# Kernel optimization log

Measured on AMD Instinct MI355X. Metric: run time of the kernel, lower is better.

Reference implementation:

```python
import jax, jax.numpy as jnp
import numpy as np

HIDDEN = 2048
NUM_HEADS = 8
NUM_KV_HEADS = 4
HEAD_DIM = 256
N_REP = NUM_HEADS // NUM_KV_HEADS
EPS = 1e-6


def setup_inputs() -> dict:
    key = jax.random.key(0)
    ks = jax.random.split(key, 5)
    B, L = 2, 2048
    hidden_states = jax.random.normal(ks[0], (B, L, HIDDEN), dtype=jnp.float32)
    q_w = jax.random.normal(ks[1], (NUM_HEADS * HEAD_DIM, HIDDEN), dtype=jnp.float32) * 0.02
    k_w = jax.random.normal(ks[2], (NUM_KV_HEADS * HEAD_DIM, HIDDEN), dtype=jnp.float32) * 0.02
    v_w = jax.random.normal(ks[3], (NUM_KV_HEADS * HEAD_DIM, HIDDEN), dtype=jnp.float32) * 0.02
    o_w = jax.random.normal(ks[4], (HIDDEN, NUM_HEADS * HEAD_DIM), dtype=jnp.float32) * 0.02
    qnorm_w = jnp.ones((HEAD_DIM,), dtype=jnp.float32)
    knorm_w = jnp.ones((HEAD_DIM,), dtype=jnp.float32)
    return {"hidden_states": hidden_states, "q_w": q_w, "k_w": k_w, "v_w": v_w,
            "o_w": o_w, "qnorm_w": qnorm_w, "knorm_w": knorm_w}


def _rmsnorm(x, w):
    # RMSNorm over last dim (head_dim)
    var = jnp.mean(jnp.square(x), axis=-1, keepdims=True)
    return x * jax.lax.rsqrt(var + EPS) * w


def reference(hidden_states, q_w, k_w, v_w, o_w, qnorm_w, knorm_w):
    B, L, H = hidden_states.shape
    scale = HEAD_DIM ** -0.5
    # projections (Linear without bias: x @ W.T)
    q = (hidden_states @ q_w.T).reshape(B, L, NUM_HEADS, HEAD_DIM)
    k = (hidden_states @ k_w.T).reshape(B, L, NUM_KV_HEADS, HEAD_DIM)
    v = (hidden_states @ v_w.T).reshape(B, L, NUM_KV_HEADS, HEAD_DIM)
    # QK-norm on head_dim
    q = _rmsnorm(q, qnorm_w)
    k = _rmsnorm(k, knorm_w)
    # [B, heads, L, d]
    q = q.transpose(0, 2, 1, 3)
    k = k.transpose(0, 2, 1, 3)
    v = v.transpose(0, 2, 1, 3)
    # GQA expand kv heads: [B, kv, L, d] -> [B, kv*n_rep, L, d]
    k = jnp.repeat(k, N_REP, axis=1)
    v = jnp.repeat(v, N_REP, axis=1)
    # scores [B, h, q, k]
    scores = jnp.einsum('bhqd,bhkd->bhqk', q, k) * scale
    causal = jnp.triu(jnp.ones((L, L), dtype=bool), k=1)
    scores = jnp.where(causal, -jnp.inf, scores)
    probs = jax.nn.softmax(scores, axis=-1)
    out = jnp.einsum('bhqk,bhkd->bhqd', probs, v)
    out = out.transpose(0, 2, 1, 3).reshape(B, L, NUM_HEADS * HEAD_DIM)
    return out @ o_w.T
```

## Files before the change

kernel.cpp:

```cpp
#include <hip/hip_runtime.h>

typedef __bf16 bf16;
typedef __attribute__((ext_vector_type(4))) float f32x4;
typedef __attribute__((ext_vector_type(8))) __bf16 bf16x8;
typedef __attribute__((ext_vector_type(4))) __bf16 bf16x4;

#define HIDDEN 2048
#define L_SEQ 2048
#define NHEADS 8
#define NKV 4
#define HDIM 256

__device__ __forceinline__ void gload16(const bf16* g, void* l) {
  __builtin_amdgcn_global_load_lds((const __attribute__((address_space(1))) void*)g,
                                   (__attribute__((address_space(3))) void*)l, 16, 0, 0);
}

__global__ __launch_bounds__(256) void cast_bf16_kernel(const float* __restrict__ in,
                                                        bf16* __restrict__ out, int n4) {
  int i = blockIdx.x * 256 + threadIdx.x;
  if (i >= n4) return;
  float4 v = ((const float4*)in)[i];
  bf16x4 o;
  o[0] = (bf16)v.x; o[1] = (bf16)v.y; o[2] = (bf16)v.z; o[3] = (bf16)v.w;
  ((bf16x4*)out)[i] = o;
}

template <int OUT_BF16>
__global__ __launch_bounds__(256) void gemm_bt(const bf16* __restrict__ A,
                                               const bf16* __restrict__ B,
                                               void* __restrict__ C,
                                               int M, int N, int K) {
  __shared__ __attribute__((aligned(16))) bf16 As[128 * 64];
  __shared__ __attribute__((aligned(16))) bf16 Bs[128 * 64];
  const int tid = threadIdx.x;
  const int lane = tid & 63;
  const int wid = tid >> 6;
  const int m0 = blockIdx.y * 128;
  const int n0 = blockIdx.x * 128;
  const int wm = (wid >> 1) * 64;
  const int wn = (wid & 1) * 64;

  const int srow = tid >> 3;
  const int scolb = (tid & 7) * 16;

  f32x4 acc[4][4];
#pragma unroll
  for (int i = 0; i < 4; ++i)
#pragma unroll
    for (int j = 0; j < 4; ++j) acc[i][j] = (f32x4){0.f, 0.f, 0.f, 0.f};

  for (int k0 = 0; k0 < K; k0 += 64) {
    __syncthreads();
#pragma unroll
    for (int c = 0; c < 4; ++c) {
      int row = c * 32 + srow;
      int gcol = (scolb ^ ((row & 7) << 4)) >> 1;
      gload16(A + (size_t)(m0 + row) * K + k0 + gcol, (char*)As + row * 128 + scolb);
      gload16(B + (size_t)(n0 + row) * K + k0 + gcol, (char*)Bs + row * 128 + scolb);
    }
    __syncthreads();
#pragma unroll
    for (int kk = 0; kk < 2; ++kk) {
      bf16x8 a[4], b[4];
      int colb = kk * 64 + (lane >> 4) * 16;
#pragma unroll
      for (int i = 0; i < 4; ++i) {
        int row = wm + i * 16 + (lane & 15);
        a[i] = *(const bf16x8*)((const char*)As + row * 128 + (colb ^ ((row & 7) << 4)));
      }
#pragma unroll
      for (int j = 0; j < 4; ++j) {
        int row = wn + j * 16 + (lane & 15);
        b[j] = *(const bf16x8*)((const char*)Bs + row * 128 + (colb ^ ((row & 7) << 4)));
      }
#pragma unroll
      for (int i = 0; i < 4; ++i)
#pragma unroll
        for (int j = 0; j < 4; ++j)
          acc[i][j] = __builtin_amdgcn_mfma_f32_16x16x32_bf16(a[i], b[j], acc[i][j], 0, 0, 0);
    }
  }
#pragma unroll
  for (int i = 0; i < 4; ++i)
#pragma unroll
    for (int j = 0; j < 4; ++j)
#pragma unroll
      for (int r = 0; r < 4; ++r) {
        int m = m0 + wm + i * 16 + ((lane >> 4) << 2) + r;
        int n = n0 + wn + j * 16 + (lane & 15);
        float v = acc[i][j][r];
        if (OUT_BF16)
          ((bf16*)C)[(size_t)m * N + n] = (bf16)v;
        else
          ((float*)C)[(size_t)m * N + n] = v;
      }
}

__global__ __launch_bounds__(256) void qknorm_kernel(const bf16* __restrict__ qkv,
                                                     const float* __restrict__ qnw,
                                                     const float* __restrict__ knw,
                                                     bf16* __restrict__ Q,
                                                     bf16* __restrict__ K,
                                                     bf16* __restrict__ Vt) {
  int w = threadIdx.x >> 6, lane = threadIdx.x & 63;
  int vec = blockIdx.x * 4 + w;
  int row = vec >> 4, sub = vec & 15;
  int b = row >> 11, l = row & 2047;
  const bf16* src = qkv + (size_t)row * 4096 + sub * 256 + lane * 4;
  bf16x4 v = *(const bf16x4*)src;
  float f[4];
#pragma unroll
  for (int j = 0; j < 4; ++j) f[j] = (float)v[j];

  if (sub < 12) {
    float ss = f[0] * f[0] + f[1] * f[1] + f[2] * f[2] + f[3] * f[3];
#pragma unroll
    for (int off = 1; off < 64; off <<= 1) ss += __shfl_xor(ss, off);
    float rs = rsqrtf(ss * (1.0f / 256.0f) + 1e-6f);
    if (sub < 8) {
      rs *= 0.0625f;
      bf16x4 o;
#pragma unroll
      for (int j = 0; j < 4; ++j) o[j] = (bf16)(f[j] * rs * qnw[lane * 4 + j]);
      *(bf16x4*)(Q + ((size_t)(b * 8 + sub) * 2048 + l) * 256 + lane * 4) = o;
    } else {
      bf16x4 o;
#pragma unroll
      for (int j = 0; j < 4; ++j) o[j] = (bf16)(f[j] * rs * knw[lane * 4 + j]);
      *(bf16x4*)(K + ((size_t)(b * 4 + (sub - 8)) * 2048 + l) * 256 + lane * 4) = o;
    }
  } else {
    bf16* dst = Vt + (size_t)(b * 4 + (sub - 12)) * 256 * 2048 + l;
#pragma unroll
    for (int j = 0; j < 4; ++j) dst[(size_t)(lane * 4 + j) * 2048] = v[j];
  }
}

__global__ __launch_bounds__(256, 1) void attn_kernel(const bf16* __restrict__ Q,
                                                      const bf16* __restrict__ K,
                                                      const bf16* __restrict__ Vt,
                                                      bf16* __restrict__ Out) {
  extern __shared__ __attribute__((aligned(16))) char smem[];
  bf16* PL = (bf16*)(smem + 131072);

  const int tid = threadIdx.x;
  const int lane = tid & 63;
  const int w = tid >> 6;
  const int head_sub = w & 1;
  const int half = w >> 1;
  const int bid = blockIdx.x;
  const int p = bid & 31;
  const int kh = (bid >> 5) & 3;
  const int b = bid >> 7;
  const int head = kh * 2 + head_sub;
  const int l15 = lane & 15;
  const int l4 = lane >> 4;
  const int koff = l4 * 8;
  bf16* Pw = PL + w * 16 * 72;

  const bf16* Kp = K + (size_t)(b * 4 + kh) * 2048 * 256;
  const bf16* Vp = Vt + (size_t)(b * 4 + kh) * 256 * 2048;

#pragma unroll
  for (int ph = 0; ph < 2; ++ph) {
    const int t = ph ? 63 - p : p;
    const int nkb = (t >> 1) + 1;
    const int q0 = t * 32 + half * 16;

    const bf16* Qp = Q + ((size_t)(b * 8 + head) * 2048 + q0) * 256;
    bf16x8 qf[8];
#pragma unroll
    for (int c = 0; c < 8; ++c)
      qf[c] = *(const bf16x8*)(Qp + (size_t)l15 * 256 + c * 32 + koff);

    f32x4 o[16];
#pragma unroll
    for (int dt = 0; dt < 16; ++dt) o[dt] = (f32x4){0.f, 0.f, 0.f, 0.f};
    float mrow[4], lrow[4];
#pragma unroll
    for (int r = 0; r < 4; ++r) { mrow[r] = -__builtin_inff(); lrow[r] = 0.f; }

#pragma unroll
    for (int i = 0; i < 8; ++i) {
      int cid = i * 256 + tid;
      int row = cid >> 5, c = cid & 31;
      gload16(Kp + (size_t)row * 256 + ((c ^ (row & 7)) << 3), smem + cid * 16);
    }
#pragma unroll
    for (int i = 0; i < 8; ++i) {
      int cid = i * 256 + tid;
      int row = cid >> 3, c = cid & 7;
      gload16(Vp + (size_t)row * 2048 + ((c ^ (row & 7)) << 3), smem + 65536 + cid * 16);
    }
    __syncthreads();

    for (int kb = 0; kb < nkb; ++kb) {
      const int cur = kb & 1;
      const char* ksb = smem + cur * 32768;
      const char* vsb = smem + 65536 + cur * 32768;
      if (kb + 1 < nkb) {
        const int kv0 = (kb + 1) * 64;
        char* kd = smem + (cur ^ 1) * 32768;
        char* vd = smem + 65536 + (cur ^ 1) * 32768;
#pragma unroll
        for (int i = 0; i < 8; ++i) {
          int cid = i * 256 + tid;
          int row = cid >> 5, c = cid & 31;
          gload16(Kp + (size_t)(kv0 + row) * 256 + ((c ^ (row & 7)) << 3), kd + cid * 16);
        }
#pragma unroll
        for (int i = 0; i < 8; ++i) {
          int cid = i * 256 + tid;
          int row = cid >> 3, c = cid & 7;
          gload16(Vp + (size_t)row * 2048 + kv0 + ((c ^ (row & 7)) << 3), vd + cid * 16);
        }
      }

      f32x4 s[4];
#pragma unroll
      for (int kt = 0; kt < 4; ++kt) s[kt] = (f32x4){0.f, 0.f, 0.f, 0.f};
#pragma unroll
      for (int kt = 0; kt < 4; ++kt) {
        int row = kt * 16 + l15;
        const char* kr = ksb + row * 512;
        bf16x8 kf[8];
#pragma unroll
        for (int kk = 0; kk < 8; ++kk) {
          int c = (kk * 4 + l4) ^ (row & 7);
          kf[kk] = *(const bf16x8*)(kr + c * 16);
        }
#pragma unroll
        for (int kk = 0; kk < 8; ++kk)
          s[kt] = __builtin_amdgcn_mfma_f32_16x16x32_bf16(qf[kk], kf[kk], s[kt], 0, 0, 0);
      }
      if (kb == nkb - 1) {
#pragma unroll
        for (int kt = 0; kt < 4; ++kt) {
          int key = kb * 64 + kt * 16 + l15;
#pragma unroll
          for (int r = 0; r < 4; ++r) {
            int qg = q0 + (l4 << 2) + r;
            if (key > qg) s[kt][r] = -__builtin_inff();
          }
        }
      }
      float rm[4];
#pragma unroll
      for (int r = 0; r < 4; ++r) {
        float m = fmaxf(fmaxf(s[0][r], s[1][r]), fmaxf(s[2][r], s[3][r]));
#pragma unroll
        for (int off = 1; off < 16; off <<= 1) m = fmaxf(m, __shfl_xor(m, off));
        rm[r] = m;
      }
      bool small = (rm[0] - mrow[0] <= 8.f) && (rm[1] - mrow[1] <= 8.f) &&
                   (rm[2] - mrow[2] <= 8.f) && (rm[3] - mrow[3] <= 8.f);
      if (__all(small)) {
        float rsum[4] = {0.f, 0.f, 0.f, 0.f};
#pragma unroll
        for (int kt = 0; kt < 4; ++kt)
#pragma unroll
          for (int r = 0; r < 4; ++r) {
            float pe = __expf(s[kt][r] - mrow[r]);
            s[kt][r] = pe;
            rsum[r] += pe;
          }
#pragma unroll
        for (int r = 0; r < 4; ++r) {
#pragma unroll
          for (int off = 1; off < 16; off <<= 1) rsum[r] += __shfl_xor(rsum[r], off);
          lrow[r] += rsum[r];
        }
      } else {
        float mnew[4], scl[4], rsum[4];
#pragma unroll
        for (int r = 0; r < 4; ++r) {
          mnew[r] = fmaxf(mrow[r], rm[r]);
          scl[r] = __expf(mrow[r] - mnew[r]);
          rsum[r] = 0.f;
        }
#pragma unroll
        for (int kt = 0; kt < 4; ++kt)
#pragma unroll
          for (int r = 0; r < 4; ++r) {
            float pe = __expf(s[kt][r] - mnew[r]);
            s[kt][r] = pe;
            rsum[r] += pe;
          }
#pragma unroll
        for (int r = 0; r < 4; ++r) {
#pragma unroll
          for (int off = 1; off < 16; off <<= 1) rsum[r] += __shfl_xor(rsum[r], off);
          lrow[r] = lrow[r] * scl[r] + rsum[r];
          mrow[r] = mnew[r];
        }
#pragma unroll
        for (int dt = 0; dt < 16; ++dt)
#pragma unroll
          for (int r = 0; r < 4; ++r) o[dt][r] *= scl[r];
      }
#pragma unroll
      for (int kt = 0; kt < 4; ++kt)
#pragma unroll
        for (int r = 0; r < 4; ++r)
          Pw[((l4 << 2) + r) * 72 + kt * 16 + l15] = (bf16)s[kt][r];
      bf16x8 pa[2];
#pragma unroll
      for (int kk2 = 0; kk2 < 2; ++kk2)
        pa[kk2] = *(const bf16x8*)&Pw[l15 * 72 + kk2 * 32 + koff];
#pragma unroll
      for (int g = 0; g < 4; ++g) {
        bf16x8 vf[8];
#pragma unroll
        for (int tt = 0; tt < 4; ++tt) {
          int row = (g * 4 + tt) * 16 + l15;
          const char* vr = vsb + row * 128;
          int c0 = l4 ^ (row & 7);
          int c1 = (4 + l4) ^ (row & 7);
          vf[tt * 2] = *(const bf16x8*)(vr + c0 * 16);
          vf[tt * 2 + 1] = *(const bf16x8*)(vr + c1 * 16);
        }
#pragma unroll
        for (int tt = 0; tt < 4; ++tt) {
          int dt = g * 4 + tt;
          o[dt] = __builtin_amdgcn_mfma_f32_16x16x32_bf16(pa[0], vf[tt * 2], o[dt], 0, 0, 0);
          o[dt] = __builtin_amdgcn_mfma_f32_16x16x32_bf16(pa[1], vf[tt * 2 + 1], o[dt], 0, 0, 0);
        }
      }
      __syncthreads();
    }
    float rcp[4];
#pragma unroll
    for (int r = 0; r < 4; ++r) rcp[r] = 1.0f / lrow[r];
#pragma unroll
    for (int dt = 0; dt < 16; ++dt)
#pragma unroll
      for (int r = 0; r < 4; ++r) {
        int qg = q0 + (l4 << 2) + r;
        Out[(size_t)(b * 2048 + qg) * 2048 + head * 256 + dt * 16 + l15] =
            (bf16)(o[dt][r] * rcp[r]);
      }
  }
}

extern "C" void kernel_launch(void* const* d_in, const int* in_sizes, int n_in,
                              void* d_out, int out_size, void* d_ws, size_t ws_size,
                              hipStream_t stream) {
  const float* hidden = (const float*)d_in[0];
  const float* q_w = (const float*)d_in[1];
  const float* k_w = (const float*)d_in[2];
  const float* v_w = (const float*)d_in[3];
  const float* o_w = (const float*)d_in[4];
  const float* qnw = (const float*)d_in[5];
  const float* knw = (const float*)d_in[6];

  char* ws = (char*)d_ws;
  const size_t MB = (size_t)1 << 20;
  bf16* h_bf  = (bf16*)(ws + 0 * MB);
  bf16* wqkv  = (bf16*)(ws + 16 * MB);
  bf16* wo    = (bf16*)(ws + 32 * MB);
  bf16* qkv   = (bf16*)(ws + 40 * MB);
  bf16* aout  = qkv;
  bf16* Qb    = (bf16*)(ws + 72 * MB);
  bf16* Kb    = (bf16*)(ws + 88 * MB);
  bf16* Vt    = (bf16*)(ws + 96 * MB);

  cast_bf16_kernel<<<8192, 256, 0, stream>>>(hidden, h_bf, 2097152);
  cast_bf16_kernel<<<4096, 256, 0, stream>>>(q_w, wqkv, 1048576);
  cast_bf16_kernel<<<2048, 256, 0, stream>>>(k_w, wqkv + (size_t)2048 * 2048, 524288);
  cast_bf16_kernel<<<2048, 256, 0, stream>>>(v_w, wqkv + (size_t)3072 * 2048, 524288);
  cast_bf16_kernel<<<4096, 256, 0, stream>>>(o_w, wo, 1048576);

  gemm_bt<1><<<dim3(32, 32), 256, 0, stream>>>(h_bf, wqkv, qkv, 4096, 4096, 2048);
  qknorm_kernel<<<16384, 256, 0, stream>>>(qkv, qnw, knw, Qb, Kb, Vt);

  static const int ATTN_LDS = 140288;
  (void)hipFuncSetAttribute((const void*)attn_kernel,
                            hipFuncAttributeMaxDynamicSharedMemorySize, ATTN_LDS);
  attn_kernel<<<256, 256, ATTN_LDS, stream>>>(Qb, Kb, Vt, aout);

  gemm_bt<0><<<dim3(16, 32), 256, 0, stream>>>(aout, wo, d_out, 4096, 2048, 2048);
}
```

Baseline: 428.3 us.

## Replace double-buffered K/V prefetch in attention with single-buffered synchronous loads

Attention now uses one K/V LDS buffer per iteration instead of two. Each iteration issues the loads for the current block, then waits for them to complete behind an explicit waitcnt and barrier before computing, so LDS shrinks from about 137KB to 73KB. The launch keeps __launch_bounds__(256,1) and a 256-block grid, so occupancy probably does not rise, and load latency is no longer hidden behind MFMA work.

```diff
diff --git a/kernel.cpp b/kernel.cpp
--- a/kernel.cpp
+++ b/kernel.cpp
@@ -14,6 +14,13 @@
 __device__ __forceinline__ void gload16(const bf16* g, void* l) {
   __builtin_amdgcn_global_load_lds((const __attribute__((address_space(1))) void*)g,
                                    (__attribute__((address_space(3))) void*)l, 16, 0, 0);
+}
+
+__device__ __forceinline__ void hard_barrier() {
+  __builtin_amdgcn_sched_barrier(0);
+  asm volatile("s_waitcnt vmcnt(0) lgkmcnt(0)" ::: "memory");
+  __builtin_amdgcn_s_barrier();
+  __builtin_amdgcn_sched_barrier(0);
 }
 
 __global__ __launch_bounds__(256) void cast_bf16_kernel(const float* __restrict__ in,
@@ -142,7 +149,7 @@
                                                       const bf16* __restrict__ Vt,
                                                       bf16* __restrict__ Out) {
   extern __shared__ __attribute__((aligned(16))) char smem[];
-  bf16* PL = (bf16*)(smem + 131072);
+  bf16* PL = (bf16*)(smem + 65536);
 
   const int tid = threadIdx.x;
   const int lane = tid & 63;
@@ -181,41 +188,23 @@
 #pragma unroll
     for (int r = 0; r < 4; ++r) { mrow[r] = -__builtin_inff(); lrow[r] = 0.f; }
 
-#pragma unroll
-    for (int i = 0; i < 8; ++i) {
-      int cid = i * 256 + tid;
-      int row = cid >> 5, c = cid & 31;
-      gload16(Kp + (size_t)row * 256 + ((c ^ (row & 7)) << 3), smem + cid * 16);
-    }
-#pragma unroll
-    for (int i = 0; i < 8; ++i) {
-      int cid = i * 256 + tid;
-      int row = cid >> 3, c = cid & 7;
-      gload16(Vp + (size_t)row * 2048 + ((c ^ (row & 7)) << 3), smem + 65536 + cid * 16);
-    }
-    __syncthreads();
-
     for (int kb = 0; kb < nkb; ++kb) {
-      const int cur = kb & 1;
-      const char* ksb = smem + cur * 32768;
-      const char* vsb = smem + 65536 + cur * 32768;
-      if (kb + 1 < nkb) {
-        const int kv0 = (kb + 1) * 64;
-        char* kd = smem + (cur ^ 1) * 32768;
-        char* vd = smem + 65536 + (cur ^ 1) * 32768;
-#pragma unroll
-        for (int i = 0; i < 8; ++i) {
-          int cid = i * 256 + tid;
-          int row = cid >> 5, c = cid & 31;
-          gload16(Kp + (size_t)(kv0 + row) * 256 + ((c ^ (row & 7)) << 3), kd + cid * 16);
-        }
-#pragma unroll
-        for (int i = 0; i < 8; ++i) {
-          int cid = i * 256 + tid;
-          int row = cid >> 3, c = cid & 7;
-          gload16(Vp + (size_t)row * 2048 + kv0 + ((c ^ (row & 7)) << 3), vd + cid * 16);
-        }
-      }
+      hard_barrier();
+      const int kv0 = kb * 64;
+#pragma unroll
+      for (int i = 0; i < 8; ++i) {
+        int cid = i * 256 + tid;
+        int row = cid >> 5, c = cid & 31;
+        gload16(Kp + (size_t)(kv0 + row) * 256 + ((c ^ (row & 7)) << 3), smem + cid * 16);
+      }
+#pragma unroll
+      for (int i = 0; i < 8; ++i) {
+        int cid = i * 256 + tid;
+        int row = cid >> 3, c = cid & 7;
+        gload16(Vp + (size_t)row * 2048 + kv0 + ((c ^ (row & 7)) << 3),
+                smem + 32768 + cid * 16);
+      }
+      hard_barrier();
 
       f32x4 s[4];
 #pragma unroll
@@ -223,7 +212,7 @@
 #pragma unroll
       for (int kt = 0; kt < 4; ++kt) {
         int row = kt * 16 + l15;
-        const char* kr = ksb + row * 512;
+        const char* kr = smem + row * 512;
         bf16x8 kf[8];
 #pragma unroll
         for (int kk = 0; kk < 8; ++kk) {
@@ -314,7 +303,7 @@
 #pragma unroll
         for (int tt = 0; tt < 4; ++tt) {
           int row = (g * 4 + tt) * 16 + l15;
-          const char* vr = vsb + row * 128;
+          const char* vr = smem + 32768 + row * 128;
           int c0 = l4 ^ (row & 7);
           int c1 = (4 + l4) ^ (row & 7);
           vf[tt * 2] = *(const bf16x8*)(vr + c0 * 16);
@@ -327,7 +316,6 @@
           o[dt] = __builtin_amdgcn_mfma_f32_16x16x32_bf16(pa[1], vf[tt * 2 + 1], o[dt], 0, 0, 0);
         }
       }
-      __syncthreads();
     }
     float rcp[4];
 #pragma unroll
@@ -374,7 +362,7 @@
   gemm_bt<1><<<dim3(32, 32), 256, 0, stream>>>(h_bf, wqkv, qkv, 4096, 4096, 2048);
   qknorm_kernel<<<16384, 256, 0, stream>>>(qkv, qnw, knw, Qb, Kb, Vt);
 
-  static const int ATTN_LDS = 140288;
+  static const int ATTN_LDS = 74752;
   (void)hipFuncSetAttribute((const void*)attn_kernel,
                             hipFuncAttributeMaxDynamicSharedMemorySize, ATTN_LDS);
   attn_kernel<<<256, 256, ATTN_LDS, stream>>>(Qb, Kb, Vt, aout);
```

Measured after the change: 454.6 us. +6.1%, slower.
